# Performance work log

Hardware: AMD Instinct MI355X
Metric: run time of the kernel (lower is better)

Reference implementation:

```python
import jax, jax.numpy as jnp
import numpy as np

BATCH = 1048576
D_IN = 4        # d_in=3 spatial dims + 1 time dim
HID = 64
N_HID_STACK = 4  # hidden residual blocks after the first hidden layer
D_OUT = 3
BN_EPS = 1e-5


def _bn(x, gamma, beta):
    # BatchNorm1d in training mode: biased batch statistics over the batch axis
    mu = jnp.mean(x, axis=0)
    var = jnp.var(x, axis=0)
    return gamma * (x - mu) * jax.lax.rsqrt(var + BN_EPS) + beta


def setup_inputs() -> dict:
    key = jax.random.key(0)
    ks = jax.random.split(key, 8)
    s_in = 1.0 / np.sqrt(D_IN)
    s_h = 1.0 / np.sqrt(HID)
    return {
        "x": jax.random.normal(ks[0], (BATCH, D_IN), dtype=jnp.float32),
        "bn0_gamma": jnp.ones((D_IN,), jnp.float32),
        "bn0_beta": jnp.zeros((D_IN,), jnp.float32),
        "W0": jax.random.normal(ks[1], (D_IN, HID), jnp.float32) * s_in,
        "b0": jnp.zeros((HID,), jnp.float32),
        "gamma0": jnp.ones((HID,), jnp.float32),
        "beta0": jnp.zeros((HID,), jnp.float32),
        "W_hid": jax.random.normal(ks[2], (N_HID_STACK, HID, HID), jnp.float32) * s_h,
        "b_hid": jnp.zeros((N_HID_STACK, HID), jnp.float32),
        "gamma_hid": jnp.ones((N_HID_STACK, HID), jnp.float32),
        "beta_hid": jnp.zeros((N_HID_STACK, HID), jnp.float32),
        "Wout": jax.random.normal(ks[3], (HID, D_OUT), jnp.float32) * s_h,
        "bout": jnp.zeros((D_OUT,), jnp.float32),
    }


def reference(x, bn0_gamma, bn0_beta, W0, b0, gamma0, beta0,
              W_hid, b_hid, gamma_hid, beta_hid, Wout, bout):
    # Net.forward (u-network, single patch, batch_normalization=True, tanh):
    #   x = bn0(x)
    #   y = bn(act(Linear0(x)))                 (first hidden layer, no skip)
    #   y = bn_i(act(Linear_i(y))) + y          (residual hidden layers)
    #   y = Linear_out(y)
    h = _bn(x, bn0_gamma, bn0_beta)
    y = _bn(jnp.tanh(h @ W0 + b0), gamma0, beta0)

    def step(y, layer):
        W, b, g, be = layer
        return _bn(jnp.tanh(y @ W + b), g, be) + y, None

    y, _ = jax.lax.scan(step, y, (W_hid, b_hid, gamma_hid, beta_hid))
    return y @ Wout + bout
```

## Files before the change

kernel.cpp:

```cpp
#include <hip/hip_runtime.h>
#include <stdint.h>


#define NROWS 1048576
#define EPS 1e-5f
#define INV_B 9.5367431640625e-07f
#define LOG2E2 2.885390081777927f
#define BIGGRID 16384
#define NBUCKET 256

typedef __attribute__((ext_vector_type(8))) short bfrag;
typedef __attribute__((ext_vector_type(4))) float facc;
typedef __attribute__((ext_vector_type(4))) float f4v;
typedef unsigned int u32;

__device__ __forceinline__ float bf2f(short s) {
  union { unsigned u; float f; } v;
  v.u = ((unsigned)(unsigned short)s) << 16;
  return v.f;
}
__device__ __forceinline__ short f2bf(float f) {
  union { float f; unsigned u; } v;
  v.f = f;
  unsigned r = v.u + 0x7FFFu + ((v.u >> 16) & 1u);
  return (short)(r >> 16);
}
__device__ __forceinline__ unsigned cvt_pk_bf16(float lo, float hi) {
  unsigned r;
  asm("v_cvt_pk_bf16_f32 %0, %1, %2" : "=v"(r) : "v"(lo), "v"(hi));
  return r;
}
__device__ __forceinline__ float tanh_fast(float x) {
  float e = __builtin_amdgcn_exp2f(x * LOG2E2);
  return 1.f - 2.f * __builtin_amdgcn_rcpf(e + 1.f);
}
__device__ __forceinline__ void gld16(const void* g, void* l) {
  __builtin_amdgcn_global_load_lds(
      (const __attribute__((address_space(1))) u32*)g,
      (__attribute__((address_space(3))) u32*)l, 16, 0, 0);
}
__device__ __forceinline__ int ysw(int r, int c) {
  return (r << 6) + ((((c >> 3) ^ (r & 7)) << 3) | (c & 7));
}

template <int W>
__global__ __launch_bounds__(256) void k_reduce(const float* __restrict__ P,
                                                float* __restrict__ S,
                                                int rows_per_blk) {
  __shared__ float red[256];
  const int tid = threadIdx.x;
  const int col = tid % W;
  const int grp = tid / W;
  const int G = 256 / W;
  size_t r0 = (size_t)blockIdx.x * rows_per_blk;
  float s = 0.f;
  for (int r = grp; r < rows_per_blk; r += G) s += P[(r0 + r) * W + col];
  red[tid] = s;
  __syncthreads();
  if (tid < W) {
    float t = 0.f;
#pragma unroll 4
    for (int g = 0; g < G; ++g) t += red[g * W + tid];
    atomicAdd(&S[tid], t);
  }
}


__global__ __launch_bounds__(256) void k_stats_x(const float* __restrict__ x,
                                                 const float* __restrict__ Wh,
                                                 short* __restrict__ WT,
                                                 float* __restrict__ P) {
  __shared__ float red[4][8];
  const int tid = threadIdx.x;
  const int wave = tid >> 6;
  const int bid = blockIdx.x;

  if (bid < 64) {
    int idx = bid * 256 + tid;
    int l = idx >> 12, rem = idx & 4095, k = rem >> 6, c = rem & 63;
    WT[l * 4096 + c * 64 + k] = f2bf(Wh[l * 4096 + k * 64 + c]);
  }

  size_t base = (size_t)bid * 1024 + tid;
  float s[4] = {0.f, 0.f, 0.f, 0.f}, q[4] = {0.f, 0.f, 0.f, 0.f};
#pragma unroll
  for (int it = 0; it < 4; ++it) {
    f4v v = *(const f4v*)(x + (base + (size_t)it * 256) * 4);
#pragma unroll
    for (int k = 0; k < 4; ++k) { s[k] += v[k]; q[k] = fmaf(v[k], v[k], q[k]); }
  }
#pragma unroll
  for (int off = 32; off > 0; off >>= 1) {
#pragma unroll
    for (int k = 0; k < 4; ++k) {
      s[k] += __shfl_xor(s[k], off);
      q[k] += __shfl_xor(q[k], off);
    }
  }
  if ((tid & 63) == 0) {
#pragma unroll
    for (int k = 0; k < 4; ++k) { red[wave][k] = s[k]; red[wave][4 + k] = q[k]; }
  }
  __syncthreads();
  if (tid < 8)
    P[bid * 8 + tid] = red[0][tid] + red[1][tid] + red[2][tid] + red[3][tid];
}

__global__ __launch_bounds__(256) void k_stats_z1(
    const float* __restrict__ x, const float* __restrict__ bn0g,
    const float* __restrict__ bn0b, const float* __restrict__ W0,
    const float* __restrict__ b0, const float* __restrict__ sx,
    float* __restrict__ P) {
  __shared__ float red[2][4][64];
  const int tid = threadIdx.x;
  const int lane = tid & 63;
  const int wave = tid >> 6;
  int gw = blockIdx.x * 4 + wave;
  float sc[4], sh[4];
#pragma unroll
  for (int k = 0; k < 4; ++k) {
    float mean = sx[k] * INV_B;
    float var = fmaf(-mean, mean, sx[4 + k] * INV_B);
    float rs = rsqrtf(var + EPS);
    sc[k] = bn0g[k] * rs;
    sh[k] = fmaf(-sc[k], mean, bn0b[k]);
  }
  float w2[4];
  float b2 = b0[lane];
#pragma unroll
  for (int k = 0; k < 4; ++k) {
    float w = W0[k * 64 + lane];
    w2[k] = sc[k] * w;
    b2 = fmaf(sh[k], w, b2);
  }
  float s = 0.f, q = 0.f;
  size_t r0 = (size_t)gw * 128;
  for (int r = 0; r < 128; ++r) {
    f4v xv = *(const f4v*)(x + (r0 + r) * 4);
    float acc = b2;
#pragma unroll
    for (int k = 0; k < 4; ++k) acc = fmaf(xv[k], w2[k], acc);
    float z = tanh_fast(acc);
    s += z;
    q = fmaf(z, z, q);
  }
  red[0][wave][lane] = s;
  red[1][wave][lane] = q;
  __syncthreads();
  if (tid < 128) {
    int which = tid >> 6, c = tid & 63;
    P[blockIdx.x * 128 + tid] = red[which][0][c] + red[which][1][c] +
                                red[which][2][c] + red[which][3][c];
  }
}


__global__ __launch_bounds__(128) void k_first(
    const float* __restrict__ x, const float* __restrict__ bn0g,
    const float* __restrict__ bn0b, const float* __restrict__ W0,
    const float* __restrict__ b0, const float* __restrict__ gamma0,
    const float* __restrict__ beta0, const float* __restrict__ sx,
    const float* __restrict__ s1, const short* __restrict__ WTb,
    const float* __restrict__ bb, float* __restrict__ Pb,
    short* __restrict__ Y) {
  __shared__ __align__(16) float lds_x[64 * 4];
  __shared__ __align__(16) short lds_y[64 * 72];
  __shared__ float red[2][128];

  const int tid = threadIdx.x;
  const int lane = tid & 63;
  const int wave = tid >> 6;
  const int l15 = lane & 15;
  const int q = lane >> 4;
  const int wr = wave * 32;
  const size_t r0 = (size_t)blockIdx.x * 64;

  f4v xp;
  if (lane < 32) xp = *(const f4v*)(x + (r0 + wr + lane) * 4);

  float sc0[4], sh0[4];
#pragma unroll
  for (int k = 0; k < 4; ++k) {
    float mean = sx[k] * INV_B;
    float var = fmaf(-mean, mean, sx[4 + k] * INV_B);
    float rs = rsqrtf(var + EPS);
    sc0[k] = bn0g[k] * rs;
    sh0[k] = fmaf(-sc0[k], mean, bn0b[k]);
  }
  float w2[4];
  float b2 = b0[lane];
#pragma unroll
  for (int k = 0; k < 4; ++k) {
    float w = W0[k * 64 + lane];
    w2[k] = sc0[k] * w;
    b2 = fmaf(sh0[k], w, b2);
  }
  float mean1 = s1[lane] * INV_B;
  float var1 = fmaf(-mean1, mean1, s1[64 + lane] * INV_B);
  float A1c = gamma0[lane] * rsqrtf(var1 + EPS);
  float B1c = fmaf(-A1c, mean1, beta0[lane]);
  if (lane < 32) *(f4v*)&lds_x[(wr + lane) * 4] = xp;

  for (int e = 0; e < 32; e += 2) {
    int row = wr + e;
    f4v xv0 = *(const f4v*)&lds_x[row * 4];
    f4v xv1 = *(const f4v*)&lds_x[(row + 1) * 4];
    float a0 = b2, a1 = b2;
#pragma unroll
    for (int k = 0; k < 4; ++k) {
      a0 = fmaf(xv0[k], w2[k], a0);
      a1 = fmaf(xv1[k], w2[k], a1);
    }
    float z0 = tanh_fast(a0), z1 = tanh_fast(a1);
    unsigned p = cvt_pk_bf16(fmaf(A1c, z0, B1c), fmaf(A1c, z1, B1c));
    lds_y[row * 72 + lane] = (short)p;
    lds_y[(row + 1) * 72 + lane] = (short)(p >> 16);
  }

  bfrag af[2][2];
#pragma unroll
  for (int mt = 0; mt < 2; ++mt)
#pragma unroll
    for (int kt = 0; kt < 2; ++kt) {
      af[mt][kt] =
          *(const bfrag*)&lds_y[(wr + mt * 16 + l15) * 72 + kt * 32 + q * 8];
      *(bfrag*)(Y + (r0 + wr + mt * 16 + l15) * 64 + kt * 32 + q * 8) =
          af[mt][kt];
    }
  float bbv[4];
  bfrag bwb[4][2];
#pragma unroll
  for (int nt = 0; nt < 4; ++nt) {
    bbv[nt] = bb[nt * 16 + l15];
#pragma unroll
    for (int kt = 0; kt < 2; ++kt)
      bwb[nt][kt] =
          *(const bfrag*)(WTb + (nt * 16 + l15) * 64 + kt * 32 + q * 8);
  }
  facc acc2[2][4];
#pragma unroll
  for (int mt = 0; mt < 2; ++mt)
#pragma unroll
    for (int nt = 0; nt < 4; ++nt) {
      acc2[mt][nt][0] = bbv[nt]; acc2[mt][nt][1] = bbv[nt];
      acc2[mt][nt][2] = bbv[nt]; acc2[mt][nt][3] = bbv[nt];
    }
#pragma unroll
  for (int mt = 0; mt < 2; ++mt)
#pragma unroll
    for (int nt = 0; nt < 4; ++nt)
#pragma unroll
      for (int kt = 0; kt < 2; ++kt)
        acc2[mt][nt] = __builtin_amdgcn_mfma_f32_16x16x32_bf16(
            af[mt][kt], bwb[nt][kt], acc2[mt][nt], 0, 0, 0);
#pragma unroll
  for (int nt = 0; nt < 4; ++nt) {
    float s = 0.f, ss = 0.f;
#pragma unroll
    for (int mt = 0; mt < 2; ++mt)
#pragma unroll
      for (int i = 0; i < 4; ++i) {
        float z = tanh_fast(acc2[mt][nt][i]);
        s += z;
        ss = fmaf(z, z, ss);
      }
    s += __shfl_xor(s, 16); s += __shfl_xor(s, 32);
    ss += __shfl_xor(ss, 16); ss += __shfl_xor(ss, 32);
    if (q == 0) {
      red[wave][nt * 16 + l15] = s;
      red[wave][64 + nt * 16 + l15] = ss;
    }
  }
  __syncthreads();
  atomicAdd(&Pb[(size_t)(blockIdx.x & (NBUCKET - 1)) * 128 + tid],
            red[0][tid] + red[1][tid]);
}

__global__ __launch_bounds__(128) void k_mid(
    short* __restrict__ Y, const short* __restrict__ WTa,
    const float* __restrict__ ba, const float* __restrict__ ga,
    const float* __restrict__ bea, const float* __restrict__ sa,
    const short* __restrict__ WTb, const float* __restrict__ bb,
    float* __restrict__ Pb) {
  __shared__ __align__(16) short lds_y[64 * 64];
  __shared__ float red[2][128];

  const int tid = threadIdx.x;
  const int lane = tid & 63;
  const int wave = tid >> 6;
  const int l15 = lane & 15;
  const int q = lane >> 4;
  const int wr = wave * 32;
  const size_t r0 = (size_t)blockIdx.x * 64;

  {
    const int srow = lane >> 3;
    const int cu = ((lane & 7) ^ srow) * 8;
#pragma unroll
    for (int it = 0; it < 4; ++it)
      gld16(Y + (r0 + wr + it * 8 + srow) * 64 + cu,
            &lds_y[(wr + it * 8) * 64]);
  }

  float Av[4], Bv[4], bav[4];
#pragma unroll
  for (int nt = 0; nt < 4; ++nt) {
    int c = nt * 16 + l15;
    float mean = sa[c] * INV_B;
    float var = fmaf(-mean, mean, sa[64 + c] * INV_B);
    float A = ga[c] * rsqrtf(var + EPS);
    Av[nt] = A;
    Bv[nt] = fmaf(-A, mean, bea[c]);
    bav[nt] = ba[c];
  }
  bfrag bwa[4][2];
#pragma unroll
  for (int nt = 0; nt < 4; ++nt)
#pragma unroll
    for (int kt = 0; kt < 2; ++kt)
      bwa[nt][kt] =
          *(const bfrag*)(WTa + (nt * 16 + l15) * 64 + kt * 32 + q * 8);

  asm volatile("s_waitcnt vmcnt(0)" ::: "memory");

  bfrag af[2][2];
#pragma unroll
  for (int mt = 0; mt < 2; ++mt)
#pragma unroll
    for (int kt = 0; kt < 2; ++kt)
      af[mt][kt] =
          *(const bfrag*)&lds_y[ysw(wr + mt * 16 + l15, kt * 32 + q * 8)];
  facc acc[2][4];
#pragma unroll
  for (int mt = 0; mt < 2; ++mt)
#pragma unroll
    for (int nt = 0; nt < 4; ++nt) {
      acc[mt][nt][0] = bav[nt]; acc[mt][nt][1] = bav[nt];
      acc[mt][nt][2] = bav[nt]; acc[mt][nt][3] = bav[nt];
    }
#pragma unroll
  for (int mt = 0; mt < 2; ++mt)
#pragma unroll
    for (int nt = 0; nt < 4; ++nt)
#pragma unroll
      for (int kt = 0; kt < 2; ++kt)
        acc[mt][nt] = __builtin_amdgcn_mfma_f32_16x16x32_bf16(
            af[mt][kt], bwa[nt][kt], acc[mt][nt], 0, 0, 0);

#pragma unroll
  for (int mt = 0; mt < 2; ++mt)
#pragma unroll
    for (int nt = 0; nt < 4; ++nt) {
      int c = nt * 16 + l15;
      float A = Av[nt], Bc = Bv[nt];
      int rb = wr + mt * 16 + q * 4;
      float v0 = fmaf(A, tanh_fast(acc[mt][nt][0]), Bc) +
                 bf2f(lds_y[ysw(rb + 0, c)]);
      float v1 = fmaf(A, tanh_fast(acc[mt][nt][1]), Bc) +
                 bf2f(lds_y[ysw(rb + 1, c)]);
      float v2 = fmaf(A, tanh_fast(acc[mt][nt][2]), Bc) +
                 bf2f(lds_y[ysw(rb + 2, c)]);
      float v3 = fmaf(A, tanh_fast(acc[mt][nt][3]), Bc) +
                 bf2f(lds_y[ysw(rb + 3, c)]);
      unsigned p01 = cvt_pk_bf16(v0, v1);
      unsigned p23 = cvt_pk_bf16(v2, v3);
      lds_y[ysw(rb + 0, c)] = (short)p01;
      lds_y[ysw(rb + 1, c)] = (short)(p01 >> 16);
      lds_y[ysw(rb + 2, c)] = (short)p23;
      lds_y[ysw(rb + 3, c)] = (short)(p23 >> 16);
    }

#pragma unroll
  for (int mt = 0; mt < 2; ++mt)
#pragma unroll
    for (int kt = 0; kt < 2; ++kt) {
      af[mt][kt] =
          *(const bfrag*)&lds_y[ysw(wr + mt * 16 + l15, kt * 32 + q * 8)];
      *(bfrag*)(Y + (r0 + wr + mt * 16 + l15) * 64 + kt * 32 + q * 8) =
          af[mt][kt];
    }
  float bbv[4];
  bfrag bwb[4][2];
#pragma unroll
  for (int nt = 0; nt < 4; ++nt) {
    bbv[nt] = bb[nt * 16 + l15];
#pragma unroll
    for (int kt = 0; kt < 2; ++kt)
      bwb[nt][kt] =
          *(const bfrag*)(WTb + (nt * 16 + l15) * 64 + kt * 32 + q * 8);
  }
#pragma unroll
  for (int mt = 0; mt < 2; ++mt)
#pragma unroll
    for (int nt = 0; nt < 4; ++nt) {
      acc[mt][nt][0] = bbv[nt]; acc[mt][nt][1] = bbv[nt];
      acc[mt][nt][2] = bbv[nt]; acc[mt][nt][3] = bbv[nt];
    }
#pragma unroll
  for (int mt = 0; mt < 2; ++mt)
#pragma unroll
    for (int nt = 0; nt < 4; ++nt)
#pragma unroll
      for (int kt = 0; kt < 2; ++kt)
        acc[mt][nt] = __builtin_amdgcn_mfma_f32_16x16x32_bf16(
            af[mt][kt], bwb[nt][kt], acc[mt][nt], 0, 0, 0);
#pragma unroll
  for (int nt = 0; nt < 4; ++nt) {
    float s = 0.f, ss = 0.f;
#pragma unroll
    for (int mt = 0; mt < 2; ++mt)
#pragma unroll
      for (int i = 0; i < 4; ++i) {
        float z = tanh_fast(acc[mt][nt][i]);
        s += z;
        ss = fmaf(z, z, ss);
      }
    s += __shfl_xor(s, 16); s += __shfl_xor(s, 32);
    ss += __shfl_xor(ss, 16); ss += __shfl_xor(ss, 32);
    if (q == 0) {
      red[wave][nt * 16 + l15] = s;
      red[wave][64 + nt * 16 + l15] = ss;
    }
  }
  __syncthreads();
  atomicAdd(&Pb[(size_t)(blockIdx.x & (NBUCKET - 1)) * 128 + tid],
            red[0][tid] + red[1][tid]);
}

__global__ __launch_bounds__(128) void k_last(
    const short* __restrict__ Y, const short* __restrict__ WTa,
    const float* __restrict__ ba, const float* __restrict__ ga,
    const float* __restrict__ bea, const float* __restrict__ sa,
    const float* __restrict__ Wout, const float* __restrict__ bout,
    float* __restrict__ out) {
  __shared__ __align__(16) short lds_y[64 * 64];
  __shared__ float lds_wo[192];

  const int tid = threadIdx.x;
  const int lane = tid & 63;
  const int wave = tid >> 6;
  const int l15 = lane & 15;
  const int q = lane >> 4;
  const int wr = wave * 32;
  const size_t r0 = (size_t)blockIdx.x * 64;

  {
    const int srow = lane >> 3;
    const int cu = ((lane & 7) ^ srow) * 8;
#pragma unroll
    for (int it = 0; it < 4; ++it)
      gld16(Y + (r0 + wr + it * 8 + srow) * 64 + cu,
            &lds_y[(wr + it * 8) * 64]);
  }

  for (int i = tid; i < 192; i += 128) lds_wo[i] = Wout[i];
  float Av[4], Bv[4], bav[4];
#pragma unroll
  for (int nt = 0; nt < 4; ++nt) {
    int c = nt * 16 + l15;
    float mean = sa[c] * INV_B;
    float var = fmaf(-mean, mean, sa[64 + c] * INV_B);
    float A = ga[c] * rsqrtf(var + EPS);
    Av[nt] = A;
    Bv[nt] = fmaf(-A, mean, bea[c]);
    bav[nt] = ba[c];
  }
  bfrag bwa[4][2];
#pragma unroll
  for (int nt = 0; nt < 4; ++nt)
#pragma unroll
    for (int kt = 0; kt < 2; ++kt)
      bwa[nt][kt] =
          *(const bfrag*)(WTa + (nt * 16 + l15) * 64 + kt * 32 + q * 8);
  float bo0 = bout[0], bo1 = bout[1], bo2 = bout[2];

  asm volatile("s_waitcnt vmcnt(0)" ::: "memory");
  __syncthreads();

  bfrag af[2][2];
#pragma unroll
  for (int mt = 0; mt < 2; ++mt)
#pragma unroll
    for (int kt = 0; kt < 2; ++kt)
      af[mt][kt] =
          *(const bfrag*)&lds_y[ysw(wr + mt * 16 + l15, kt * 32 + q * 8)];
  facc acc[2][4];
#pragma unroll
  for (int mt = 0; mt < 2; ++mt)
#pragma unroll
    for (int nt = 0; nt < 4; ++nt) {
      acc[mt][nt][0] = bav[nt]; acc[mt][nt][1] = bav[nt];
      acc[mt][nt][2] = bav[nt]; acc[mt][nt][3] = bav[nt];
    }
#pragma unroll
  for (int mt = 0; mt < 2; ++mt)
#pragma unroll
    for (int nt = 0; nt < 4; ++nt)
#pragma unroll
      for (int kt = 0; kt < 2; ++kt)
        acc[mt][nt] = __builtin_amdgcn_mfma_f32_16x16x32_bf16(
            af[mt][kt], bwa[nt][kt], acc[mt][nt], 0, 0, 0);
#pragma unroll
  for (int mt = 0; mt < 2; ++mt)
#pragma unroll
    for (int nt = 0; nt < 4; ++nt) {
      int c = nt * 16 + l15;
      float A = Av[nt], Bc = Bv[nt];
      int rb = wr + mt * 16 + q * 4;
      float v0 = fmaf(A, tanh_fast(acc[mt][nt][0]), Bc) +
                 bf2f(lds_y[ysw(rb + 0, c)]);
      float v1 = fmaf(A, tanh_fast(acc[mt][nt][1]), Bc) +
                 bf2f(lds_y[ysw(rb + 1, c)]);
      float v2 = fmaf(A, tanh_fast(acc[mt][nt][2]), Bc) +
                 bf2f(lds_y[ysw(rb + 2, c)]);
      float v3 = fmaf(A, tanh_fast(acc[mt][nt][3]), Bc) +
                 bf2f(lds_y[ysw(rb + 3, c)]);
      unsigned p01 = cvt_pk_bf16(v0, v1);
      unsigned p23 = cvt_pk_bf16(v2, v3);
      lds_y[ysw(rb + 0, c)] = (short)p01;
      lds_y[ysw(rb + 1, c)] = (short)(p01 >> 16);
      lds_y[ysw(rb + 2, c)] = (short)p23;
      lds_y[ysw(rb + 3, c)] = (short)(p23 >> 16);
    }

  {
    int row = wr + (lane >> 1);
    int cb = (lane & 1) * 32;
    float o0 = 0.f, o1 = 0.f, o2 = 0.f;
#pragma unroll
    for (int jc = 0; jc < 4; ++jc) {
      bfrag v = *(const bfrag*)&lds_y[ysw(row, cb + jc * 8)];
#pragma unroll
      for (int j = 0; j < 8; ++j) {
        float f = bf2f(v[j]);
        int jj = cb + jc * 8 + j;
        o0 = fmaf(f, lds_wo[jj * 3 + 0], o0);
        o1 = fmaf(f, lds_wo[jj * 3 + 1], o1);
        o2 = fmaf(f, lds_wo[jj * 3 + 2], o2);
      }
    }
    o0 += __shfl_xor(o0, 1);
    o1 += __shfl_xor(o1, 1);
    o2 += __shfl_xor(o2, 1);
    if ((lane & 1) == 0) {
      size_t ro = (r0 + row) * 3;
      out[ro] = o0 + bo0;
      out[ro + 1] = o1 + bo1;
      out[ro + 2] = o2 + bo2;
    }
  }
}

extern "C" void kernel_launch(void* const* d_in, const int* in_sizes, int n_in,
                              void* d_out, int out_size, void* d_ws,
                              size_t ws_size, hipStream_t stream) {
  (void)in_sizes; (void)n_in; (void)out_size; (void)ws_size;
  const float* x = (const float*)d_in[0];
  const float* bn0g = (const float*)d_in[1];
  const float* bn0b = (const float*)d_in[2];
  const float* W0 = (const float*)d_in[3];
  const float* b0 = (const float*)d_in[4];
  const float* gamma0 = (const float*)d_in[5];
  const float* beta0 = (const float*)d_in[6];
  const float* Wh = (const float*)d_in[7];
  const float* bh = (const float*)d_in[8];
  const float* gh = (const float*)d_in[9];
  const float* beh = (const float*)d_in[10];
  const float* Wout = (const float*)d_in[11];
  const float* bout = (const float*)d_in[12];
  float* out = (float*)d_out;

  char* ws = (char*)d_ws;
  short* Y = (short*)ws;
  const size_t YB = (size_t)NROWS * 64 * 2;
  float* stats = (float*)(ws + YB);
  float* Sx = stats;
  float* S1 = stats + 8;
  float* S2 = stats + 136;
  float* S3 = stats + 264;
  float* S4 = stats + 392;
  float* S5 = stats + 520;
  float* Pb2 = stats + 648;
  float* Pb3 = Pb2 + NBUCKET * 128;
  float* Pb4 = Pb3 + NBUCKET * 128;
  float* Pb5 = Pb4 + NBUCKET * 128;
  const size_t zbytes = (648 + 4 * NBUCKET * 128) * sizeof(float);
  short* WT = (short*)(ws + YB + ((zbytes + 255) & ~(size_t)255));
  float* P = (float*)((char*)WT + 32768);

  hipMemsetAsync(stats, 0, zbytes, stream);
  k_stats_x<<<1024, 256, 0, stream>>>(x, Wh, WT, P);
  k_reduce<8><<<8, 256, 0, stream>>>(P, Sx, 128);
  k_stats_z1<<<2048, 256, 0, stream>>>(x, bn0g, bn0b, W0, b0, Sx, P);
  k_reduce<128><<<16, 256, 0, stream>>>(P, S1, 128);
  k_first<<<BIGGRID, 128, 0, stream>>>(x, bn0g, bn0b, W0, b0, gamma0, beta0,
                                       Sx, S1, WT, bh, Pb2, Y);
  k_reduce<128><<<16, 256, 0, stream>>>(Pb2, S2, 16);
  k_mid<<<BIGGRID, 128, 0, stream>>>(Y, WT, bh, gh, beh, S2, WT + 4096,
                                     bh + 64, Pb3);
  k_reduce<128><<<16, 256, 0, stream>>>(Pb3, S3, 16);
  k_mid<<<BIGGRID, 128, 0, stream>>>(Y, WT + 4096, bh + 64, gh + 64, beh + 64,
                                     S3, WT + 2 * 4096, bh + 128, Pb4);
  k_reduce<128><<<16, 256, 0, stream>>>(Pb4, S4, 16);
  k_mid<<<BIGGRID, 128, 0, stream>>>(Y, WT + 2 * 4096, bh + 128, gh + 128,
                                     beh + 128, S4, WT + 3 * 4096, bh + 192,
                                     Pb5);
  k_reduce<128><<<16, 256, 0, stream>>>(Pb5, S5, 16);
  k_last<<<BIGGRID, 128, 0, stream>>>(Y, WT + 3 * 4096, bh + 192, gh + 192,
                                      beh + 192, S5, Wout, bout, out);
}
```

Before: 490.8 us.

## Process two 64-row tiles per block to halve grid and amortize setup

```diff
diff --git a/kernel.cpp b/kernel.cpp
--- a/kernel.cpp
+++ b/kernel.cpp
@@ -6,7 +6,7 @@
 #define EPS 1e-5f
 #define INV_B 9.5367431640625e-07f
 #define LOG2E2 2.885390081777927f
-#define BIGGRID 16384
+#define BIGGRID 8192
 #define NBUCKET 256
 
 typedef __attribute__((ext_vector_type(8))) short bfrag;
@@ -163,7 +163,7 @@
     const float* __restrict__ s1, const short* __restrict__ WTb,
     const float* __restrict__ bb, float* __restrict__ Pb,
     short* __restrict__ Y) {
-  __shared__ __align__(16) float lds_x[64 * 4];
+  __shared__ __align__(16) float lds_x[2][64 * 4];
   __shared__ __align__(16) short lds_y[64 * 72];
   __shared__ float red[2][128];
 
@@ -173,10 +173,13 @@
   const int l15 = lane & 15;
   const int q = lane >> 4;
   const int wr = wave * 32;
-  const size_t r0 = (size_t)blockIdx.x * 64;
-
-  f4v xp;
-  if (lane < 32) xp = *(const f4v*)(x + (r0 + wr + lane) * 4);
+  const size_t r0 = (size_t)blockIdx.x * 128;
+
+  if (lane < 32) {
+#pragma unroll
+    for (int b = 0; b < 2; ++b)
+      gld16(x + (r0 + b * 64 + wr + lane) * 4, &lds_x[b][wr * 4]);
+  }
 
   float sc0[4], sh0[4];
 #pragma unroll
@@ -199,34 +202,6 @@
   float var1 = fmaf(-mean1, mean1, s1[64 + lane] * INV_B);
   float A1c = gamma0[lane] * rsqrtf(var1 + EPS);
   float B1c = fmaf(-A1c, mean1, beta0[lane]);
-  if (lane < 32) *(f4v*)&lds_x[(wr + lane) * 4] = xp;
-
-  for (int e = 0; e < 32; e += 2) {
-    int row = wr + e;
-    f4v xv0 = *(const f4v*)&lds_x[row * 4];
-    f4v xv1 = *(const f4v*)&lds_x[(row + 1) * 4];
-    float a0 = b2, a1 = b2;
-#pragma unroll
-    for (int k = 0; k < 4; ++k) {
-      a0 = fmaf(xv0[k], w2[k], a0);
-      a1 = fmaf(xv1[k], w2[k], a1);
-    }
-    float z0 = tanh_fast(a0), z1 = tanh_fast(a1);
-    unsigned p = cvt_pk_bf16(fmaf(A1c, z0, B1c), fmaf(A1c, z1, B1c));
-    lds_y[row * 72 + lane] = (short)p;
-    lds_y[(row + 1) * 72 + lane] = (short)(p >> 16);
-  }
-
-  bfrag af[2][2];
-#pragma unroll
-  for (int mt = 0; mt < 2; ++mt)
-#pragma unroll
-    for (int kt = 0; kt < 2; ++kt) {
-      af[mt][kt] =
-          *(const bfrag*)&lds_y[(wr + mt * 16 + l15) * 72 + kt * 32 + q * 8];
-      *(bfrag*)(Y + (r0 + wr + mt * 16 + l15) * 64 + kt * 32 + q * 8) =
-          af[mt][kt];
-    }
   float bbv[4];
   bfrag bwb[4][2];
 #pragma unroll
@@ -237,38 +212,75 @@
       bwb[nt][kt] =
           *(const bfrag*)(WTb + (nt * 16 + l15) * 64 + kt * 32 + q * 8);
   }
-  facc acc2[2][4];
-#pragma unroll
-  for (int mt = 0; mt < 2; ++mt)
+  asm volatile("s_waitcnt vmcnt(0)" ::: "memory");
+
+#pragma unroll
+  for (int b = 0; b < 2; ++b) {
+    const size_t rb = r0 + b * 64;
+    for (int e = 0; e < 32; e += 2) {
+      int row = wr + e;
+      f4v xv0 = *(const f4v*)&lds_x[b][row * 4];
+      f4v xv1 = *(const f4v*)&lds_x[b][(row + 1) * 4];
+      float a0 = b2, a1 = b2;
+#pragma unroll
+      for (int k = 0; k < 4; ++k) {
+        a0 = fmaf(xv0[k], w2[k], a0);
+        a1 = fmaf(xv1[k], w2[k], a1);
+      }
+      float z0 = tanh_fast(a0), z1 = tanh_fast(a1);
+      unsigned p = cvt_pk_bf16(fmaf(A1c, z0, B1c), fmaf(A1c, z1, B1c));
+      lds_y[row * 72 + lane] = (short)p;
+      lds_y[(row + 1) * 72 + lane] = (short)(p >> 16);
+    }
+
+    bfrag af[2][2];
+#pragma unroll
+    for (int mt = 0; mt < 2; ++mt)
+#pragma unroll
+      for (int kt = 0; kt < 2; ++kt) {
+        af[mt][kt] =
+            *(const bfrag*)&lds_y[(wr + mt * 16 + l15) * 72 + kt * 32 + q * 8];
+        *(bfrag*)(Y + (rb + wr + mt * 16 + l15) * 64 + kt * 32 + q * 8) =
+            af[mt][kt];
+      }
+    facc acc2[2][4];
+#pragma unroll
+    for (int mt = 0; mt < 2; ++mt)
+#pragma unroll
+      for (int nt = 0; nt < 4; ++nt) {
+        acc2[mt][nt][0] = bbv[nt]; acc2[mt][nt][1] = bbv[nt];
+        acc2[mt][nt][2] = bbv[nt]; acc2[mt][nt][3] = bbv[nt];
+      }
+#pragma unroll
+    for (int mt = 0; mt < 2; ++mt)
+#pragma unroll
+      for (int nt = 0; nt < 4; ++nt)
+#pragma unroll
+        for (int kt = 0; kt < 2; ++kt)
+          acc2[mt][nt] = __builtin_amdgcn_mfma_f32_16x16x32_bf16(
+              af[mt][kt], bwb[nt][kt], acc2[mt][nt], 0, 0, 0);
 #pragma unroll
     for (int nt = 0; nt < 4; ++nt) {
-      acc2[mt][nt][0] = bbv[nt]; acc2[mt][nt][1] = bbv[nt];
-      acc2[mt][nt][2] = bbv[nt]; acc2[mt][nt][3] = bbv[nt];
-    }
-#pragma unroll
-  for (int mt = 0; mt < 2; ++mt)
-#pragma unroll
-    for (int nt = 0; nt < 4; ++nt)
-#pragma unroll
-      for (int kt = 0; kt < 2; ++kt)
-        acc2[mt][nt] = __builtin_amdgcn_mfma_f32_16x16x32_bf16(
-            af[mt][kt], bwb[nt][kt], acc2[mt][nt], 0, 0, 0);
-#pragma unroll
-  for (int nt = 0; nt < 4; ++nt) {
-    float s = 0.f, ss = 0.f;
-#pragma unroll
-    for (int mt = 0; mt < 2; ++mt)
-#pragma unroll
-      for (int i = 0; i < 4; ++i) {
-        float z = tanh_fast(acc2[mt][nt][i]);
-        s += z;
-        ss = fmaf(z, z, ss);
-      }
-    s += __shfl_xor(s, 16); s += __shfl_xor(s, 32);
-    ss += __shfl_xor(ss, 16); ss += __shfl_xor(ss, 32);
-    if (q == 0) {
-      red[wave][nt * 16 + l15] = s;
-      red[wave][64 + nt * 16 + l15] = ss;
+      float s = 0.f, ss = 0.f;
+#pragma unroll
+      for (int mt = 0; mt < 2; ++mt)
+#pragma unroll
+        for (int i = 0; i < 4; ++i) {
+          float z = tanh_fast(acc2[mt][nt][i]);
+          s += z;
+          ss = fmaf(z, z, ss);
+        }
+      s += __shfl_xor(s, 16); s += __shfl_xor(s, 32);
+      ss += __shfl_xor(ss, 16); ss += __shfl_xor(ss, 32);
+      if (q == 0) {
+        if (b == 0) {
+          red[wave][nt * 16 + l15] = s;
+          red[wave][64 + nt * 16 + l15] = ss;
+        } else {
+          red[wave][nt * 16 + l15] += s;
+          red[wave][64 + nt * 16 + l15] += ss;
+        }
+      }
     }
   }
   __syncthreads();
@@ -282,7 +294,7 @@
     const float* __restrict__ bea, const float* __restrict__ sa,
     const short* __restrict__ WTb, const float* __restrict__ bb,
     float* __restrict__ Pb) {
-  __shared__ __align__(16) short lds_y[64 * 64];
+  __shared__ __align__(16) short lds_y[2][64 * 64];
   __shared__ float red[2][128];
 
   const int tid = threadIdx.x;
@@ -291,15 +303,17 @@
   const int l15 = lane & 15;
   const int q = lane >> 4;
   const int wr = wave * 32;
-  const size_t r0 = (size_t)blockIdx.x * 64;
+  const size_t r0 = (size_t)blockIdx.x * 128;
 
   {
     const int srow = lane >> 3;
     const int cu = ((lane & 7) ^ srow) * 8;
 #pragma unroll
-    for (int it = 0; it < 4; ++it)
-      gld16(Y + (r0 + wr + it * 8 + srow) * 64 + cu,
-            &lds_y[(wr + it * 8) * 64]);
+    for (int b = 0; b < 2; ++b)
+#pragma unroll
+      for (int it = 0; it < 4; ++it)
+        gld16(Y + (r0 + b * 64 + wr + it * 8 + srow) * 64 + cu,
+              &lds_y[b][(wr + it * 8) * 64]);
   }
 
   float Av[4], Bv[4], bav[4];
@@ -323,103 +337,114 @@
 
   asm volatile("s_waitcnt vmcnt(0)" ::: "memory");
 
-  bfrag af[2][2];
-#pragma unroll
-  for (int mt = 0; mt < 2; ++mt)
-#pragma unroll
-    for (int kt = 0; kt < 2; ++kt)
-      af[mt][kt] =
-          *(const bfrag*)&lds_y[ysw(wr + mt * 16 + l15, kt * 32 + q * 8)];
-  facc acc[2][4];
-#pragma unroll
-  for (int mt = 0; mt < 2; ++mt)
+#pragma unroll
+  for (int b = 0; b < 2; ++b) {
+    short* cur = &lds_y[b][0];
+    const size_t rb = r0 + b * 64;
+
+    bfrag af[2][2];
+#pragma unroll
+    for (int mt = 0; mt < 2; ++mt)
+#pragma unroll
+      for (int kt = 0; kt < 2; ++kt)
+        af[mt][kt] =
+            *(const bfrag*)&cur[ysw(wr + mt * 16 + l15, kt * 32 + q * 8)];
+    facc acc[2][4];
+#pragma unroll
+    for (int mt = 0; mt < 2; ++mt)
+#pragma unroll
+      for (int nt = 0; nt < 4; ++nt) {
+        acc[mt][nt][0] = bav[nt]; acc[mt][nt][1] = bav[nt];
+        acc[mt][nt][2] = bav[nt]; acc[mt][nt][3] = bav[nt];
+      }
+#pragma unroll
+    for (int mt = 0; mt < 2; ++mt)
+#pragma unroll
+      for (int nt = 0; nt < 4; ++nt)
+#pragma unroll
+        for (int kt = 0; kt < 2; ++kt)
+          acc[mt][nt] = __builtin_amdgcn_mfma_f32_16x16x32_bf16(
+              af[mt][kt], bwa[nt][kt], acc[mt][nt], 0, 0, 0);
+
+#pragma unroll
+    for (int mt = 0; mt < 2; ++mt)
+#pragma unroll
+      for (int nt = 0; nt < 4; ++nt) {
+        int c = nt * 16 + l15;
+        float A = Av[nt], Bc = Bv[nt];
+        int rbr = wr + mt * 16 + q * 4;
+        float v0 = fmaf(A, tanh_fast(acc[mt][nt][0]), Bc) +
+                   bf2f(cur[ysw(rbr + 0, c)]);
+        float v1 = fmaf(A, tanh_fast(acc[mt][nt][1]), Bc) +
+                   bf2f(cur[ysw(rbr + 1, c)]);
+        float v2 = fmaf(A, tanh_fast(acc[mt][nt][2]), Bc) +
+                   bf2f(cur[ysw(rbr + 2, c)]);
+        float v3 = fmaf(A, tanh_fast(acc[mt][nt][3]), Bc) +
+                   bf2f(cur[ysw(rbr + 3, c)]);
+        unsigned p01 = cvt_pk_bf16(v0, v1);
+        unsigned p23 = cvt_pk_bf16(v2, v3);
+        cur[ysw(rbr + 0, c)] = (short)p01;
+        cur[ysw(rbr + 1, c)] = (short)(p01 >> 16);
+        cur[ysw(rbr + 2, c)] = (short)p23;
+        cur[ysw(rbr + 3, c)] = (short)(p23 >> 16);
+      }
+
+#pragma unroll
+    for (int mt = 0; mt < 2; ++mt)
+#pragma unroll
+      for (int kt = 0; kt < 2; ++kt) {
+        af[mt][kt] =
+            *(const bfrag*)&cur[ysw(wr + mt * 16 + l15, kt * 32 + q * 8)];
+        *(bfrag*)(Y + (rb + wr + mt * 16 + l15) * 64 + kt * 32 + q * 8) =
+            af[mt][kt];
+      }
+    float bbv[4];
+    bfrag bwb[4][2];
 #pragma unroll
     for (int nt = 0; nt < 4; ++nt) {
-      acc[mt][nt][0] = bav[nt]; acc[mt][nt][1] = bav[nt];
-      acc[mt][nt][2] = bav[nt]; acc[mt][nt][3] = bav[nt];
+      bbv[nt] = bb[nt * 16 + l15];
+#pragma unroll
+      for (int kt = 0; kt < 2; ++kt)
+        bwb[nt][kt] =
+            *(const bfrag*)(WTb + (nt * 16 + l15) * 64 + kt * 32 + q * 8);
     }
 #pragma unroll
-  for (int mt = 0; mt < 2; ++mt)
-#pragma unroll
-    for (int nt = 0; nt < 4; ++nt)
-#pragma unroll
-      for (int kt = 0; kt < 2; ++kt)
-        acc[mt][nt] = __builtin_amdgcn_mfma_f32_16x16x32_bf16(
-            af[mt][kt], bwa[nt][kt], acc[mt][nt], 0, 0, 0);
-
-#pragma unroll
-  for (int mt = 0; mt < 2; ++mt)
+    for (int mt = 0; mt < 2; ++mt)
+#pragma unroll
+      for (int nt = 0; nt < 4; ++nt) {
+        acc[mt][nt][0] = bbv[nt]; acc[mt][nt][1] = bbv[nt];
+        acc[mt][nt][2] = bbv[nt]; acc[mt][nt][3] = bbv[nt];
+      }
+#pragma unroll
+    for (int mt = 0; mt < 2; ++mt)
+#pragma unroll
+      for (int nt = 0; nt < 4; ++nt)
+#pragma unroll
+        for (int kt = 0; kt < 2; ++kt)
+          acc[mt][nt] = __builtin_amdgcn_mfma_f32_16x16x32_bf16(
+              af[mt][kt], bwb[nt][kt], acc[mt][nt], 0, 0, 0);
 #pragma unroll
     for (int nt = 0; nt < 4; ++nt) {
-      int c = nt * 16 + l15;
-      float A = Av[nt], Bc = Bv[nt];
-      int rb = wr + mt * 16 + q * 4;
-      float v0 = fmaf(A, tanh_fast(acc[mt][nt][0]), Bc) +
-                 bf2f(lds_y[ysw(rb + 0, c)]);
-      float v1 = fmaf(A, tanh_fast(acc[mt][nt][1]), Bc) +
-                 bf2f(lds_y[ysw(rb + 1, c)]);
-      float v2 = fmaf(A, tanh_fast(acc[mt][nt][2]), Bc) +
-                 bf2f(lds_y[ysw(rb + 2, c)]);
-      float v3 = fmaf(A, tanh_fast(acc[mt][nt][3]), Bc) +
-                 bf2f(lds_y[ysw(rb + 3, c)]);
-      unsigned p01 = cvt_pk_bf16(v0, v1);
-      unsigned p23 = cvt_pk_bf16(v2, v3);
-      lds_y[ysw(rb + 0, c)] = (short)p01;
-      lds_y[ysw(rb + 1, c)] = (short)(p01 >> 16);
-      lds_y[ysw(rb + 2, c)] = (short)p23;
-      lds_y[ysw(rb + 3, c)] = (short)(p23 >> 16);
-    }
-
-#pragma unroll
-  for (int mt = 0; mt < 2; ++mt)
-#pragma unroll
-    for (int kt = 0; kt < 2; ++kt) {
-      af[mt][kt] =
-          *(const bfrag*)&lds_y[ysw(wr + mt * 16 + l15, kt * 32 + q * 8)];
-      *(bfrag*)(Y + (r0 + wr + mt * 16 + l15) * 64 + kt * 32 + q * 8) =
-          af[mt][kt];
-    }
-  float bbv[4];
-  bfrag bwb[4][2];
-#pragma unroll
-  for (int nt = 0; nt < 4; ++nt) {
-    bbv[nt] = bb[nt * 16 + l15];
-#pragma unroll
-    for (int kt = 0; kt < 2; ++kt)
-      bwb[nt][kt] =
-          *(const bfrag*)(WTb + (nt * 16 + l15) * 64 + kt * 32 + q * 8);
-  }
-#pragma unroll
-  for (int mt = 0; mt < 2; ++mt)
-#pragma unroll
-    for (int nt = 0; nt < 4; ++nt) {
-      acc[mt][nt][0] = bbv[nt]; acc[mt][nt][1] = bbv[nt];
-      acc[mt][nt][2] = bbv[nt]; acc[mt][nt][3] = bbv[nt];
-    }
-#pragma unroll
-  for (int mt = 0; mt < 2; ++mt)
-#pragma unroll
-    for (int nt = 0; nt < 4; ++nt)
-#pragma unroll
-      for (int kt = 0; kt < 2; ++kt)
-        acc[mt][nt] = __builtin_amdgcn_mfma_f32_16x16x32_bf16(
-            af[mt][kt], bwb[nt][kt], acc[mt][nt], 0, 0, 0);
-#pragma unroll
-  for (int nt = 0; nt < 4; ++nt) {
-    float s = 0.f, ss = 0.f;
-#pragma unroll
-    for (int mt = 0; mt < 2; ++mt)
-#pragma unroll
-      for (int i = 0; i < 4; ++i) {
-        float z = tanh_fast(acc[mt][nt][i]);
-        s += z;
-        ss = fmaf(z, z, ss);
-      }
-    s += __shfl_xor(s, 16); s += __shfl_xor(s, 32);
-    ss += __shfl_xor(ss, 16); ss += __shfl_xor(ss, 32);
-    if (q == 0) {
-      red[wave][nt * 16 + l15] = s;
-      red[wave][64 + nt * 16 + l15] = ss;
+      float s = 0.f, ss = 0.f;
+#pragma unroll
+      for (int mt = 0; mt < 2; ++mt)
+#pragma unroll
+        for (int i = 0; i < 4; ++i) {
+          float z = tanh_fast(acc[mt][nt][i]);
+          s += z;
+          ss = fmaf(z, z, ss);
+        }
+      s += __shfl_xor(s, 16); s += __shfl_xor(s, 32);
+      ss += __shfl_xor(ss, 16); ss += __shfl_xor(ss, 32);
+      if (q == 0) {
+        if (b == 0) {
+          red[wave][nt * 16 + l15] = s;
+          red[wave][64 + nt * 16 + l15] = ss;
+        } else {
+          red[wave][nt * 16 + l15] += s;
+          red[wave][64 + nt * 16 + l15] += ss;
+        }
+      }
     }
   }
   __syncthreads();
@@ -433,7 +458,7 @@
     const float* __restrict__ bea, const float* __restrict__ sa,
     const float* __restrict__ Wout, const float* __restrict__ bout,
     float* __restrict__ out) {
-  __shared__ __align__(16) short lds_y[64 * 64];
+  __shared__ __align__(16) short lds_y[2][64 * 64];
   __shared__ float lds_wo[192];
 
   const int tid = threadIdx.x;
@@ -442,15 +467,17 @@
   const int l15 = lane & 15;
   const int q = lane >> 4;
   const int wr = wave * 32;
-  const size_t r0 = (size_t)blockIdx.x * 64;
+  const size_t r0 = (size_t)blockIdx.x * 128;
 
   {
     const int srow = lane >> 3;
     const int cu = ((lane & 7) ^ srow) * 8;
 #pragma unroll
-    for (int it = 0; it < 4; ++it)
-      gld16(Y + (r0 + wr + it * 8 + srow) * 64 + cu,
-            &lds_y[(wr + it * 8) * 64]);
+    for (int b = 0; b < 2; ++b)
+#pragma unroll
+      for (int it = 0; it < 4; ++it)
+        gld16(Y + (r0 + b * 64 + wr + it * 8 + srow) * 64 + cu,
+              &lds_y[b][(wr + it * 8) * 64]);
   }
 
   for (int i = tid; i < 192; i += 128) lds_wo[i] = Wout[i];
@@ -477,76 +504,82 @@
   asm volatile("s_waitcnt vmcnt(0)" ::: "memory");
   __syncthreads();
 
-  bfrag af[2][2];
-#pragma unroll
-  for (int mt = 0; mt < 2; ++mt)
-#pragma unroll
-    for (int kt = 0; kt < 2; ++kt)
-      af[mt][kt] =
-          *(const bfrag*)&lds_y[ysw(wr + mt * 16 + l15, kt * 32 + q * 8)];
-  facc acc[2][4];
-#pragma unroll
-  for (int mt = 0; mt < 2; ++mt)
-#pragma unroll
-    for (int nt = 0; nt < 4; ++nt) {
-      acc[mt][nt][0] = bav[nt]; acc[mt][nt][1] = bav[nt];
-      acc[mt][nt][2] = bav[nt]; acc[mt][nt][3] = bav[nt];
-    }
-#pragma unroll
-  for (int mt = 0; mt < 2; ++mt)
-#pragma unroll
-    for (int nt = 0; nt < 4; ++nt)
+#pragma unroll
+  for (int b = 0; b < 2; ++b) {
+    short* cur = &lds_y[b][0];
+    const size_t rb = r0 + b * 64;
+
+    bfrag af[2][2];
+#pragma unroll
+    for (int mt = 0; mt < 2; ++mt)
 #pragma unroll
       for (int kt = 0; kt < 2; ++kt)
-        acc[mt][nt] = __builtin_amdgcn_mfma_f32_16x16x32_bf16(
-            af[mt][kt], bwa[nt][kt], acc[mt][nt], 0, 0, 0);
-#pragma unroll
-  for (int mt = 0; mt < 2; ++mt)
-#pragma unroll
-    for (int nt = 0; nt < 4; ++nt) {
-      int c = nt * 16 + l15;
-      float A = Av[nt], Bc = Bv[nt];
-      int rb = wr + mt * 16 + q * 4;
-      float v0 = fmaf(A, tanh_fast(acc[mt][nt][0]), Bc) +
-                 bf2f(lds_y[ysw(rb + 0, c)]);
-      float v1 = fmaf(A, tanh_fast(acc[mt][nt][1]), Bc) +
-                 bf2f(lds_y[ysw(rb + 1, c)]);
-      float v2 = fmaf(A, tanh_fast(acc[mt][nt][2]), Bc) +
-                 bf2f(lds_y[ysw(rb + 2, c)]);
-      float v3 = fmaf(A, tanh_fast(acc[mt][nt][3]), Bc) +
-                 bf2f(lds_y[ysw(rb + 3, c)]);
-      unsigned p01 = cvt_pk_bf16(v0, v1);
-      unsigned p23 = cvt_pk_bf16(v2, v3);
-      lds_y[ysw(rb + 0, c)] = (short)p01;
-      lds_y[ysw(rb + 1, c)] = (short)(p01 >> 16);
-      lds_y[ysw(rb + 2, c)] = (short)p23;
-      lds_y[ysw(rb + 3, c)] = (short)(p23 >> 16);
-    }
-
-  {
-    int row = wr + (lane >> 1);
-    int cb = (lane & 1) * 32;
-    float o0 = 0.f, o1 = 0.f, o2 = 0.f;
-#pragma unroll
-    for (int jc = 0; jc < 4; ++jc) {
-      bfrag v = *(const bfrag*)&lds_y[ysw(row, cb + jc * 8)];
-#pragma unroll
-      for (int j = 0; j < 8; ++j) {
-        float f = bf2f(v[j]);
-        int jj = cb + jc * 8 + j;
-        o0 = fmaf(f, lds_wo[jj * 3 + 0], o0);
-        o1 = fmaf(f, lds_wo[jj * 3 + 1], o1);
-        o2 = fmaf(f, lds_wo[jj * 3 + 2], o2);
-      }
-    }
-    o0 += __shfl_xor(o0, 1);
-    o1 += __shfl_xor(o1, 1);
-    o2 += __shfl_xor(o2, 1);
-    if ((lane & 1) == 0) {
-      size_t ro = (r0 + row) * 3;
-      out[ro] = o0 + bo0;
-      out[ro + 1] = o1 + bo1;
-      out[ro + 2] = o2 + bo2;
+        af[mt][kt] =
+            *(const bfrag*)&cur[ysw(wr + mt * 16 + l15, kt * 32 + q * 8)];
+    facc acc[2][4];
+#pragma unroll
+    for (int mt = 0; mt < 2; ++mt)
+#pragma unroll
+      for (int nt = 0; nt < 4; ++nt) {
+        acc[mt][nt][0] = bav[nt]; acc[mt][nt][1] = bav[nt];
+        acc[mt][nt][2] = bav[nt]; acc[mt][nt][3] = bav[nt];
+      }
+#pragma unroll
+    for (int mt = 0; mt < 2; ++mt)
+#pragma unroll
+      for (int nt = 0; nt < 4; ++nt)
+#pragma unroll
+        for (int kt = 0; kt < 2; ++kt)
+          acc[mt][nt] = __builtin_amdgcn_mfma_f32_16x16x32_bf16(
+              af[mt][kt], bwa[nt][kt], acc[mt][nt], 0, 0, 0);
+#pragma unroll
+    for (int mt = 0; mt < 2; ++mt)
+#pragma unroll
+      for (int nt = 0; nt < 4; ++nt) {
+        int c = nt * 16 + l15;
+        float A = Av[nt], Bc = Bv[nt];
+        int rbr = wr + mt * 16 + q * 4;
+        float v0 = fmaf(A, tanh_fast(acc[mt][nt][0]), Bc) +
+                   bf2f(cur[ysw(rbr + 0, c)]);
+        float v1 = fmaf(A, tanh_fast(acc[mt][nt][1]), Bc) +
+                   bf2f(cur[ysw(rbr + 1, c)]);
+        float v2 = fmaf(A, tanh_fast(acc[mt][nt][2]), Bc) +
+                   bf2f(cur[ysw(rbr + 2, c)]);
+        float v3 = fmaf(A, tanh_fast(acc[mt][nt][3]), Bc) +
+                   bf2f(cur[ysw(rbr + 3, c)]);
+        unsigned p01 = cvt_pk_bf16(v0, v1);
+        unsigned p23 = cvt_pk_bf16(v2, v3);
+        cur[ysw(rbr + 0, c)] = (short)p01;
+        cur[ysw(rbr + 1, c)] = (short)(p01 >> 16);
+        cur[ysw(rbr + 2, c)] = (short)p23;
+        cur[ysw(rbr + 3, c)] = (short)(p23 >> 16);
+      }
+
+    {
+      int row = wr + (lane >> 1);
+      int cb = (lane & 1) * 32;
+      float o0 = 0.f, o1 = 0.f, o2 = 0.f;
+#pragma unroll
+      for (int jc = 0; jc < 4; ++jc) {
+        bfrag v = *(const bfrag*)&cur[ysw(row, cb + jc * 8)];
+#pragma unroll
+        for (int j = 0; j < 8; ++j) {
+          float f = bf2f(v[j]);
+          int jj = cb + jc * 8 + j;
+          o0 = fmaf(f, lds_wo[jj * 3 + 0], o0);
+          o1 = fmaf(f, lds_wo[jj * 3 + 1], o1);
+          o2 = fmaf(f, lds_wo[jj * 3 + 2], o2);
+        }
+      }
+      o0 += __shfl_xor(o0, 1);
+      o1 += __shfl_xor(o1, 1);
+      o2 += __shfl_xor(o2, 1);
+      if ((lane & 1) == 0) {
+        size_t ro = (rb + row) * 3;
+        out[ro] = o0 + bo0;
+        out[ro + 1] = o1 + bo1;
+        out[ro + 2] = o2 + bo2;
+      }
     }
   }
 }
```

New measurement: 501.2 us. 1.02x slower.
